# Performance work log

Measured on AMD Instinct MI355X. Metric: run time of the kernel, lower is better.

Reference implementation:

```python
import jax, jax.numpy as jnp
import numpy as np

B, L, D, V, K, H, HD, FFN = 64, 512, 256, 32000, 6, 4, 64, 512

def _ln(x, g, b):
    mu = x.mean(-1, keepdims=True)
    v = ((x - mu) ** 2).mean(-1, keepdims=True)
    return (x - mu) / jnp.sqrt(v + 1e-5) * g + b

def _pool(x, mask):
    # attention pooling: last real token attends over full sequence
    lengths = mask.sum(1)
    last = jnp.maximum(lengths - 1, 0)
    q = x[jnp.arange(x.shape[0]), last]                      # [B,D]
    scores = jnp.einsum('bd,bld->bl', q, x)
    scores = jnp.where(mask, scores, -60000.0)
    a = jax.nn.softmax(scores, axis=-1)
    return jnp.einsum('bl,bld->bd', a, x)

def _expert(x, mask, ln1g, ln1b, Wqkv, bqkv, Wo, bo, ln2g, ln2b, W1, b1, W2, b2):
    # pre-LN transformer block, eval mode (dropout = identity)
    Bx, Lx, _ = x.shape
    h = _ln(x, ln1g, ln1b)
    qkv = h @ Wqkv.T + bqkv                                   # [B,L,3D]
    q, k, v = jnp.split(qkv, 3, axis=-1)
    q = q.reshape(Bx, Lx, H, HD).transpose(0, 2, 1, 3)
    k = k.reshape(Bx, Lx, H, HD).transpose(0, 2, 1, 3)
    v = v.reshape(Bx, Lx, H, HD).transpose(0, 2, 1, 3)
    s = jnp.einsum('bhqd,bhkd->bhqk', q, k) / jnp.sqrt(jnp.float32(HD))
    s = jnp.where(mask[:, None, None, :], s, -1e9)            # key_padding_mask
    a = jax.nn.softmax(s, axis=-1)
    o = jnp.einsum('bhqk,bhkd->bhqd', a, v).transpose(0, 2, 1, 3).reshape(Bx, Lx, D)
    x = x + o @ Wo.T + bo
    h2 = _ln(x, ln2g, ln2b)
    ff = jax.nn.gelu(h2 @ W1.T + b1, approximate=False) @ W2.T + b2
    return x + ff

def _gru(z, m, Wih, Whh, bih, bhh):
    # torch.nn.GRUCell semantics
    gi = z @ Wih.T + bih
    gh = m @ Whh.T + bhh
    ir, iz, inn = jnp.split(gi, 3, axis=-1)
    hr, hz, hn = jnp.split(gh, 3, axis=-1)
    r = jax.nn.sigmoid(ir + hr)
    u = jax.nn.sigmoid(iz + hz)
    n = jnp.tanh(inn + r * hn)
    return (1.0 - u) * n + u * m

def setup_inputs():
    key = jax.random.key(0)
    ks = jax.random.split(key, 24)
    def nrm(k, shape, s=0.02):
        return jax.random.normal(k, shape, jnp.float32) * s
    lengths = jax.random.randint(ks[0], (B,), 1, L + 1)
    mask = jnp.arange(L)[None, :] < lengths[:, None]          # prefix mask, >=1 real token
    tokens = jnp.where(mask, jax.random.randint(ks[1], (B, L), 1, V), 0)
    return dict(
        tokens=tokens, mask=mask,
        tok_emb=nrm(ks[2], (V, D)).at[0].set(0.0),            # padding_idx=0
        pos_emb=nrm(ks[3], (L, D)),
        emb_ln_g=jnp.ones((D,)), emb_ln_b=jnp.zeros((D,)),
        ln1_g=jnp.ones((K, D)), ln1_b=jnp.zeros((K, D)),
        Wqkv=nrm(ks[4], (K, 3 * D, D)), bqkv=jnp.zeros((K, 3 * D)),
        Wo=nrm(ks[5], (K, D, D)), bo=jnp.zeros((K, D)),
        ln2_g=jnp.ones((K, D)), ln2_b=jnp.zeros((K, D)),
        W1=nrm(ks[6], (K, FFN, D)), b1=jnp.zeros((K, FFN)),
        W2=nrm(ks[7], (K, D, FFN)), b2=jnp.zeros((K, D)),
        gru_Wih=nrm(ks[8], (3 * D, D)), gru_Whh=nrm(ks[9], (3 * D, D)),
        gru_bih=jnp.zeros((3 * D,)), gru_bhh=jnp.zeros((3 * D,)),
        cls_W=nrm(ks[10], (V, D)), cls_b=jnp.zeros((V,)),
    )

def reference(tokens, mask, tok_emb, pos_emb, emb_ln_g, emb_ln_b, ln1_g, ln1_b, Wqkv, bqkv, Wo, bo, ln2_g, ln2_b, W1, b1, W2, b2, gru_Wih, gru_Whh, gru_bih, gru_bhh, cls_W, cls_b):
    x = _ln(tok_emb[tokens] + pos_emb[None, :tokens.shape[1]], emb_ln_g, emb_ln_b)
    m = jnp.zeros((tokens.shape[0], D), x.dtype)
    # sequential routing / phase-1: n_iter = K, chosen = t % K for all samples, no halting
    for t in range(K):
        e = t % K
        x = _expert(x, mask, ln1_g[e], ln1_b[e], Wqkv[e], bqkv[e], Wo[e], bo[e],
                    ln2_g[e], ln2_b[e], W1[e], b1[e], W2[e], b2[e])
        z = _pool(x, mask)
        m = _gru(z, m, gru_Wih, gru_Whh, gru_bih, gru_bhh)    # GRU memory update
    return _pool(x, mask) @ cls_W.T + cls_b                   # [B, V] logits
```

## Files before the change

### kernel.cpp

```cpp
#include <hip/hip_runtime.h>
#include <hip/hip_bf16.h>

#define BB 64
#define LL 512
#define DD 256
#define VV 32000
#define KK 6
#define HH 4
#define FF 512
#define MM (BB * LL)

typedef __hip_bfloat16 bf16;
typedef unsigned short ushort_t;
typedef __attribute__((ext_vector_type(8))) __bf16 bf16x8;
typedef __attribute__((ext_vector_type(4))) float f32x4;
#define MFMA __builtin_amdgcn_mfma_f32_16x16x32_bf16

__device__ __forceinline__ ushort_t f2bfbits(float x) {
  return __builtin_bit_cast(unsigned short, (__bf16)x);
}
__device__ __forceinline__ float bf2f(ushort_t u) {
  return __uint_as_float((unsigned)u << 16);
}
__device__ __forceinline__ unsigned pkbf(float lo, float hi) {
  return (unsigned)f2bfbits(lo) | ((unsigned)f2bfbits(hi) << 16);
}
union U8 { unsigned u[4]; bf16x8 v; };

__device__ __forceinline__ void gl_lds16(const ushort_t* g, ushort_t* l) {
  __builtin_amdgcn_global_load_lds(
      (const __attribute__((address_space(1))) unsigned int*)g,
      (__attribute__((address_space(3))) unsigned int*)l, 16, 0, 0);
}

__global__ __launch_bounds__(512) void k_lensord(const int* __restrict__ tokens,
                                                 int* __restrict__ lens,
                                                 int* __restrict__ order) {
  __shared__ int L[64];
  int t = threadIdx.x;
  int b = t >> 3, seg = t & 7;
  int c = 0;
  const int* tp = tokens + b * LL + seg * 64;
  #pragma unroll
  for (int i = 0; i < 64; i++) c += (tp[i] != 0);
  c += __shfl_down(c, 4, 64);
  c += __shfl_down(c, 2, 64);
  c += __shfl_down(c, 1, 64);
  if (seg == 0) { lens[b] = c; L[b] = c; }
  __syncthreads();
  if (t < 64) {
    int len = L[t];
    int rank = 0;
    for (int i = 0; i < 64; i++) {
      int li = L[i];
      if (li > len || (li == len && i < t)) rank++;
    }
    order[rank] = t;
  }
}

__global__ __launch_bounds__(256) void k_embed4(const int* __restrict__ tokens,
                                                const float* __restrict__ tok_emb,
                                                const float* __restrict__ pos_emb,
                                                const float* __restrict__ g,
                                                const float* __restrict__ be,
                                                const float* __restrict__ g1,
                                                const float* __restrict__ b1,
                                                ushort_t* __restrict__ X,
                                                bf16* __restrict__ H) {
  int wid = threadIdx.x >> 6, lane = threadIdx.x & 63;
  int row = blockIdx.x * 4 + wid;
  int l = row & (LL - 1);
  int tok = tokens[row];
  float4 a = *reinterpret_cast<const float4*>(tok_emb + (size_t)tok * DD + lane * 4);
  float4 p = *reinterpret_cast<const float4*>(pos_emb + (size_t)l * DD + lane * 4);
  float4 v = {a.x + p.x, a.y + p.y, a.z + p.z, a.w + p.w};
  float s = v.x + v.y + v.z + v.w;
  float q = v.x * v.x + v.y * v.y + v.z * v.z + v.w * v.w;
  #pragma unroll
  for (int o = 32; o > 0; o >>= 1) { s += __shfl_xor(s, o, 64); q += __shfl_xor(q, o, 64); }
  float mu = s * (1.f / DD);
  float rstd = rsqrtf(q * (1.f / DD) - mu * mu + 1e-5f);
  float4 gv = *reinterpret_cast<const float4*>(g + lane * 4);
  float4 bv = *reinterpret_cast<const float4*>(be + lane * 4);
  float4 o4 = {(v.x - mu) * rstd * gv.x + bv.x, (v.y - mu) * rstd * gv.y + bv.y,
               (v.z - mu) * rstd * gv.z + bv.z, (v.w - mu) * rstd * gv.w + bv.w};
  ushort4 x4;
  x4.x = f2bfbits(o4.x); x4.y = f2bfbits(o4.y); x4.z = f2bfbits(o4.z); x4.w = f2bfbits(o4.w);
  *reinterpret_cast<ushort4*>(X + (size_t)row * DD + lane * 4) = x4;
  float s2 = o4.x + o4.y + o4.z + o4.w;
  float q2 = o4.x * o4.x + o4.y * o4.y + o4.z * o4.z + o4.w * o4.w;
  #pragma unroll
  for (int o = 32; o > 0; o >>= 1) { s2 += __shfl_xor(s2, o, 64); q2 += __shfl_xor(q2, o, 64); }
  float mu2 = s2 * (1.f / DD);
  float rstd2 = rsqrtf(q2 * (1.f / DD) - mu2 * mu2 + 1e-5f);
  float4 g1v = *reinterpret_cast<const float4*>(g1 + lane * 4);
  float4 b1v = *reinterpret_cast<const float4*>(b1 + lane * 4);
  ushort4 h4;
  h4.x = f2bfbits((o4.x - mu2) * rstd2 * g1v.x + b1v.x);
  h4.y = f2bfbits((o4.y - mu2) * rstd2 * g1v.y + b1v.y);
  h4.z = f2bfbits((o4.z - mu2) * rstd2 * g1v.z + b1v.z);
  h4.w = f2bfbits((o4.w - mu2) * rstd2 * g1v.w + b1v.w);
  *reinterpret_cast<ushort4*>((ushort_t*)H + (size_t)row * DD + lane * 4) = h4;
}

__global__ __launch_bounds__(256) void k_cvtall(const float* __restrict__ Wqkv,
                                                const float* __restrict__ Wo,
                                                const float* __restrict__ W1,
                                                const float* __restrict__ W2,
                                                ushort_t* __restrict__ d) {
  int i = (blockIdx.x * 256 + threadIdx.x) * 4;
  int e = i / 524288, r = i - e * 524288;
  const float* s;
  if (r < 196608)      s = Wqkv + (size_t)e * 196608 + r;
  else if (r < 262144) s = Wo + (size_t)e * 65536 + (r - 196608);
  else if (r < 393216) s = W1 + (size_t)e * 131072 + (r - 262144);
  else                 s = W2 + (size_t)e * 131072 + (r - 393216);
  float4 v = *reinterpret_cast<const float4*>(s);
  ushort4 o;
  o.x = f2bfbits(v.x); o.y = f2bfbits(v.y); o.z = f2bfbits(v.z); o.w = f2bfbits(v.w);
  *reinterpret_cast<ushort4*>(d + i) = o;
}

template <int MT, int NT, int KD, bool GELU, bool RES, bool OUTBF16, bool FUSELN, bool QKVT>
__global__ __launch_bounds__(256) void k_mgemm(const ushort_t* __restrict__ A,
                                               const ushort_t* __restrict__ Wb,
                                               const float* __restrict__ bias,
                                               const ushort_t* __restrict__ res,
                                               void* __restrict__ outp,
                                               ushort_t* __restrict__ Hout,
                                               const float* __restrict__ lng,
                                               const float* __restrict__ lnb,
                                               const int* __restrict__ lens,
                                               int Ndim) {
  constexpr int JF = (MT == 128) ? (NT / 32) : (NT / 64);
  constexpr int AR = MT / 64, BR = NT / 64;
  constexpr int L = AR + BR;
  constexpr int NK = KD / 32;
  constexpr int ASZ = 3 * MT * 32;
  int n0 = blockIdx.x * NT, m0 = blockIdx.y * MT;
  if ((m0 & (LL - 1)) >= lens[m0 >> 9]) return;
  __shared__ __align__(16) ushort_t SH[ASZ + 3 * NT * 32];
  ushort_t* As = SH;
  ushort_t* Bs = SH + ASZ;
  int t = threadIdx.x, lane = t & 63, w = t >> 6;
  int wr = (MT == 128) ? (w >> 1) * 64 : 0;
  int wc = (MT == 128) ? (w & 1) * (NT / 2) : w * (NT / 4);
  int fr = lane & 15, fg = lane >> 4;

  int ca = lane & 3;
  const ushort_t* gA[AR];
  #pragma unroll
  for (int ra = 0; ra < AR; ra++) {
    int row = ra * 64 + (t >> 2);
    gA[ra] = A + (size_t)(m0 + row) * KD + ((ca ^ ((row >> 1) & 3)) << 3);
  }
  const ushort_t* gB[BR];
  #pragma unroll
  for (int rb = 0; rb < BR; rb++) {
    int row = rb * 64 + (t >> 2);
    gB[rb] = Wb + (size_t)(n0 + row) * KD + ((ca ^ ((row >> 1) & 3)) << 3);
  }

  f32x4 acc[4][JF];
  #pragma unroll
  for (int i = 0; i < 4; i++)
    #pragma unroll
    for (int j = 0; j < JF; j++) acc[i][j] = (f32x4){0.f, 0.f, 0.f, 0.f};

  #define STAGE(bi, koff) { \
    _Pragma("unroll") for (int ra = 0; ra < AR; ra++) gl_lds16(gA[ra] + (koff), &As[(bi) * MT * 32 + ra * 2048 + w * 512]); \
    _Pragma("unroll") for (int rb = 0; rb < BR; rb++) gl_lds16(gB[rb] + (koff), &Bs[(bi) * NT * 32 + rb * 2048 + w * 512]); }

  STAGE(0, 0);
  #pragma unroll
  for (int kt = 0; kt < NK; kt++) {
    int cur = kt % 3;
    if (kt + 1 < NK) {
      STAGE((kt + 1) % 3, (kt + 1) * 32);
      asm volatile("s_waitcnt vmcnt(%0)" :: "n"(L) : "memory");
    } else {
      asm volatile("s_waitcnt vmcnt(0)" ::: "memory");
    }
    __builtin_amdgcn_s_barrier();
    __builtin_amdgcn_sched_barrier(0);
    bf16x8 af[4], bfr[JF];
    #pragma unroll
    for (int i = 0; i < 4; i++) {
      int row = wr + i * 16 + fr;
      af[i] = *reinterpret_cast<const bf16x8*>(&As[cur * MT * 32 + row * 32 + ((fg ^ ((row >> 1) & 3)) << 3)]);
    }
    #pragma unroll
    for (int j = 0; j < JF; j++) {
      int row = wc + j * 16 + fr;
      bfr[j] = *reinterpret_cast<const bf16x8*>(&Bs[cur * NT * 32 + row * 32 + ((fg ^ ((row >> 1) & 3)) << 3)]);
    }
    #pragma unroll
    for (int i = 0; i < 4; i++)
      #pragma unroll
      for (int j = 0; j < JF; j++)
        acc[i][j] = MFMA(af[i], bfr[j], acc[i][j], 0, 0, 0);
  }
  #undef STAGE

  if constexpr (QKVT) {
    if (n0 < 512) {
      #pragma unroll
      for (int i = 0; i < 4; i++) {
        int mbase = m0 + wr + i * 16 + fg * 4;
        #pragma unroll
        for (int j = 0; j < JF; j++) {
          int n = n0 + wc + j * 16 + fr;
          float bs = bias[n];
          #pragma unroll
          for (int r = 0; r < 4; r++)
            ((ushort_t*)outp)[(size_t)(mbase + r) * 512 + n] = f2bfbits(acc[i][j][r] + bs);
        }
      }
    } else {
      __syncthreads();
      #pragma unroll
      for (int i = 0; i < 4; i++) {
        #pragma unroll
        for (int j = 0; j < JF; j++) {
          int dfull = wc + j * 16 + fr;
          float bs = bias[512 + dfull];
          int kl = wr + i * 16 + fg * 4;
          #pragma unroll
          for (int r = 0; r < 4; r++)
            SH[dfull * 136 + kl + r] = f2bfbits(acc[i][j][r] + bs);
        }
      }
      __syncthreads();
      int bidx = m0 >> 9, k0 = m0 & (LL - 1);
      #pragma unroll
      for (int it = 0; it < 16; it++) {
        int g = it * 256 + t;
        int row = g >> 4, mc = g & 15;
        uint4 val = *reinterpret_cast<const uint4*>(&SH[row * 136 + mc * 8]);
        *reinterpret_cast<uint4*>(Hout + (((size_t)(bidx * 4 + (row >> 6)) * 64 + (row & 63)) << 9) + k0 + mc * 8) = val;
      }
    }
  } else if constexpr (!FUSELN) {
    #pragma unroll
    for (int i = 0; i < 4; i++) {
      int mbase = m0 + wr + i * 16 + fg * 4;
      #pragma unroll
      for (int j = 0; j < JF; j++) {
        int n = n0 + wc + j * 16 + fr;
        float bs = bias[n];
        #pragma unroll
        for (int r = 0; r < 4; r++) {
          int m = mbase + r;
          float v = acc[i][j][r] + bs;
          if (RES) v += bf2f(res[(size_t)m * Ndim + n]);
          if (GELU) v = 0.5f * v * (1.f + erff(v * 0.70710678118f));
          if (OUTBF16) ((ushort_t*)outp)[(size_t)m * Ndim + n] = f2bfbits(v);
          else         ((float*)outp)[(size_t)m * Ndim + n] = v;
        }
      }
    }
  } else {
    __shared__ float redS[4][64], redQ[4][64], lnmv[64], lnrv[64];
    float rs[4][4], rq[4][4];
    #pragma unroll
    for (int i = 0; i < 4; i++)
      #pragma unroll
      for (int r = 0; r < 4; r++) { rs[i][r] = 0.f; rq[i][r] = 0.f; }
    #pragma unroll
    for (int i = 0; i < 4; i++) {
      #pragma unroll
      for (int j = 0; j < 4; j++) {
        int n = wc + j * 16 + fr;
        float bs = bias[n];
        #pragma unroll
        for (int r = 0; r < 4; r++) {
          int m = m0 + i * 16 + fg * 4 + r;
          float v = acc[i][j][r] + bs;
          if (RES) v += bf2f(res[(size_t)m * DD + n]);
          acc[i][j][r] = v;
          ((ushort_t*)outp)[(size_t)m * DD + n] = f2bfbits(v);
          rs[i][r] += v; rq[i][r] += v * v;
        }
      }
    }
    #pragma unroll
    for (int i = 0; i < 4; i++)
      #pragma unroll
      for (int r = 0; r < 4; r++) {
        float s = rs[i][r], q = rq[i][r];
        s += __shfl_xor(s, 1, 64); q += __shfl_xor(q, 1, 64);
        s += __shfl_xor(s, 2, 64); q += __shfl_xor(q, 2, 64);
        s += __shfl_xor(s, 4, 64); q += __shfl_xor(q, 4, 64);
        s += __shfl_xor(s, 8, 64); q += __shfl_xor(q, 8, 64);
        if (fr == 0) {
          redS[w][i * 16 + fg * 4 + r] = s;
          redQ[w][i * 16 + fg * 4 + r] = q;
        }
      }
    __syncthreads();
    if (t < 64) {
      float s = redS[0][t] + redS[1][t] + redS[2][t] + redS[3][t];
      float q = redQ[0][t] + redQ[1][t] + redQ[2][t] + redQ[3][t];
      float mu = s * (1.f / DD);
      lnmv[t] = mu;
      lnrv[t] = rsqrtf(q * (1.f / DD) - mu * mu + 1e-5f);
    }
    __syncthreads();
    #pragma unroll
    for (int i = 0; i < 4; i++) {
      #pragma unroll
      for (int j = 0; j < 4; j++) {
        int n = wc + j * 16 + fr;
        float gv = lng[n], bv = lnb[n];
        #pragma unroll
        for (int r = 0; r < 4; r++) {
          int rl = i * 16 + fg * 4 + r;
          float h = (acc[i][j][r] - lnmv[rl]) * lnrv[rl] * gv + bv;
          Hout[(size_t)(m0 + rl) * DD + n] = f2bfbits(h);
        }
      }
    }
  }
}

__global__ __launch_bounds__(512) void k_mattn10(const ushort_t* __restrict__ QK,
                                                 const ushort_t* __restrict__ VT,
                                                 const int* __restrict__ lens,
                                                 const int* __restrict__ order,
                                                 ushort_t* __restrict__ O) {
  int b = order[blockIdx.z], h = blockIdx.y;
  int len = lens[b];
  int q0 = blockIdx.x * 128;
  if (q0 >= len) return;
  int t = threadIdx.x, lane = t & 63, w = t >> 6;
  int fr = lane & 15, fg = lane >> 4;
  __shared__ __align__(16) ushort_t Kh[8192];
  __shared__ __align__(16) ushort_t Vh[8192];

  int qw = q0 + w * 16;
  bool qact = qw < len;
  int q = qw + fr;

  const ushort_t* qp = QK + (size_t)(b * LL + q) * 512 + h * 64 + fg * 8;
  bf16x8 qf0 = *reinterpret_cast<const bf16x8*>(qp);
  bf16x8 qf1 = *reinterpret_cast<const bf16x8*>(qp + 32);
  const ushort_t* vbase = VT + (((size_t)(b * 4 + h) * 64) << 9);

  const float SC = 0.125f * 1.44269504f;
  f32x4 ot[4];
  #pragma unroll
  for (int df = 0; df < 4; df++) ot[df] = (f32x4){0.f, 0.f, 0.f, 0.f};
  float lsum = 0.f;

  for (int kb = 0; kb < len; kb += 128) {
    if (kb) __syncthreads();
    int lim = min(128, len - kb);
    #pragma unroll
    for (int rr = 0; rr < 2; rr++) {
      if (rr * 64 >= lim) break;
      int krow = rr * 64 + w * 8 + (lane >> 3);
      int gk = kb + krow; if (gk > len - 1) gk = len - 1;
      int ch = lane & 7;
      const ushort_t* src = QK + (size_t)(b * LL + gk) * 512 + 256 + h * 64 + ((ch ^ (krow & 7)) << 3);
      gl_lds16(src, &Kh[rr * 4096 + w * 512]);
    }
    #pragma unroll
    for (int rr = 0; rr < 2; rr++) {
      int d = rr * 32 + w * 4 + (lane >> 4);
      int ch = lane & 15;
      int sd = (d ^ (d >> 3)) & 7;
      int chs = (ch & 8) | ((ch & 7) ^ sd);
      const ushort_t* src = vbase + ((size_t)d << 9) + kb + (chs << 3);
      gl_lds16(src, &Vh[rr * 4096 + w * 512]);
    }
    __syncthreads();

    if (qact) {
      for (int kt = 0; kt < lim; kt += 64) {
        f32x4 s[4];
        __builtin_amdgcn_s_setprio(1);
        #pragma unroll
        for (int f = 0; f < 4; f++) {
          s[f] = (f32x4){0.f, 0.f, 0.f, 0.f};
          int krow = kt + f * 16 + fr;
          const ushort_t* kp0 = &Kh[krow * 64 + ((fg ^ (krow & 7)) << 3)];
          const ushort_t* kp1 = &Kh[krow * 64 + (((4 + fg) ^ (krow & 7)) << 3)];
          s[f] = MFMA(*reinterpret_cast<const bf16x8*>(kp0), qf0, s[f], 0, 0, 0);
          s[f] = MFMA(*reinterpret_cast<const bf16x8*>(kp1), qf1, s[f], 0, 0, 0);
        }
        __builtin_amdgcn_s_setprio(0);
        float ps = 0.f;
        if (lim - kt >= 64) {
          #pragma unroll
          for (int f = 0; f < 4; f++)
            #pragma unroll
            for (int r = 0; r < 4; r++) {
              float p = exp2f(s[f][r] * SC);
              s[f][r] = p; ps += p;
            }
        } else {
          int rem = lim - kt;
          #pragma unroll
          for (int f = 0; f < 4; f++)
            #pragma unroll
            for (int r = 0; r < 4; r++) {
              float p = (f * 16 + fg * 4 + r < rem) ? exp2f(s[f][r] * SC) : 0.f;
              s[f][r] = p; ps += p;
            }
        }
        ps += __shfl_xor(ps, 16, 64);
        ps += __shfl_xor(ps, 32, 64);
        lsum += ps;
        #pragma unroll
        for (int st = 0; st < 2; st++) {
          int fA = st * 2, fB = fA + 1;
          unsigned a0 = pkbf(s[fA][0], s[fA][1]), a1 = pkbf(s[fA][2], s[fA][3]);
          unsigned b0 = pkbf(s[fB][0], s[fB][1]), b1 = pkbf(s[fB][2], s[fB][3]);
          int sA = ((fg & 1) * 2) * 16 + fr;
          int sB = sA + 16;
          unsigned wa0 = __shfl(a0, sA, 64), wb0 = __shfl(b0, sA, 64);
          unsigned wa1 = __shfl(a1, sA, 64), wb1 = __shfl(b1, sA, 64);
          unsigned wa2 = __shfl(a0, sB, 64), wb2 = __shfl(b0, sB, 64);
          unsigned wa3 = __shfl(a1, sB, 64), wb3 = __shfl(b1, sB, 64);
          bool lo = fg < 2;
          U8 pf;
          pf.u[0] = lo ? wa0 : wb0; pf.u[1] = lo ? wa1 : wb1;
          pf.u[2] = lo ? wa2 : wb2; pf.u[3] = lo ? wa3 : wb3;
          int cb = (kt >> 3) + st * 4 + fg;
          __builtin_amdgcn_s_setprio(1);
          #pragma unroll
          for (int df = 0; df < 4; df++) {
            int d = df * 16 + fr;
            int sd = (d ^ (d >> 3)) & 7;
            const ushort_t* vp = &Vh[d * 128 + ((cb ^ sd) << 3)];
            ot[df] = MFMA(*reinterpret_cast<const bf16x8*>(vp), pf.v, ot[df], 0, 0, 0);
          }
          __builtin_amdgcn_s_setprio(0);
        }
      }
    }
  }

  if (q < len) {
    float linv = 1.f / lsum;
    #pragma unroll
    for (int df = 0; df < 4; df++) {
      ushort4 ov;
      ov.x = f2bfbits(ot[df][0] * linv);
      ov.y = f2bfbits(ot[df][1] * linv);
      ov.z = f2bfbits(ot[df][2] * linv);
      ov.w = f2bfbits(ot[df][3] * linv);
      *reinterpret_cast<ushort4*>(O + (size_t)(b * LL + q) * DD + h * 64 + df * 16 + fg * 4) = ov;
    }
  }
}

__device__ __forceinline__ float blk_sum(float v, float* red) {
  #pragma unroll
  for (int o = 32; o > 0; o >>= 1) v += __shfl_down(v, o, 64);
  __syncthreads();
  if ((threadIdx.x & 63) == 0) red[threadIdx.x >> 6] = v;
  __syncthreads();
  return red[0] + red[1] + red[2] + red[3];
}

__global__ __launch_bounds__(256) void k_pool(const ushort_t* __restrict__ X,
                                              const int* __restrict__ lens,
                                              bf16* __restrict__ pooled) {
  __shared__ float red[4];
  __shared__ float qs[DD];
  __shared__ float sc[LL];
  int b = blockIdx.x, t = threadIdx.x;
  int len = lens[b];
  const ushort_t* Xb = X + (size_t)b * LL * DD;
  qs[t] = bf2f(Xb[(size_t)(len - 1) * DD + t]);
  __syncthreads();
  for (int l = t; l < LL; l += 256) {
    float s = -1e30f;
    if (l < len) {
      const ushort_t* xr = Xb + (size_t)l * DD;
      float a0 = 0.f;
      #pragma unroll
      for (int k8 = 0; k8 < 32; k8++) {
        uint4 xv = *reinterpret_cast<const uint4*>(xr + k8 * 8);
        const float* qq = qs + k8 * 8;
        a0 += bf2f((ushort_t)(xv.x & 0xffff)) * qq[0] + bf2f((ushort_t)(xv.x >> 16)) * qq[1];
        a0 += bf2f((ushort_t)(xv.y & 0xffff)) * qq[2] + bf2f((ushort_t)(xv.y >> 16)) * qq[3];
        a0 += bf2f((ushort_t)(xv.z & 0xffff)) * qq[4] + bf2f((ushort_t)(xv.z >> 16)) * qq[5];
        a0 += bf2f((ushort_t)(xv.w & 0xffff)) * qq[6] + bf2f((ushort_t)(xv.w >> 16)) * qq[7];
      }
      s = a0;
    }
    sc[l] = s;
  }
  __syncthreads();
  float mx = fmaxf(sc[t], sc[t + 256]);
  #pragma unroll
  for (int off = 32; off > 0; off >>= 1) mx = fmaxf(mx, __shfl_down(mx, off, 64));
  __syncthreads();
  if ((t & 63) == 0) red[t >> 6] = mx;
  __syncthreads();
  mx = fmaxf(fmaxf(red[0], red[1]), fmaxf(red[2], red[3]));
  float e0 = (t < len) ? __expf(sc[t] - mx) : 0.f;
  float e1 = (t + 256 < len) ? __expf(sc[t + 256] - mx) : 0.f;
  float ssum = blk_sum(e0 + e1, red);
  float inv = 1.f / ssum;
  __syncthreads();
  sc[t] = e0 * inv; sc[t + 256] = e1 * inv;
  __syncthreads();
  float acc = 0.f;
  for (int l = 0; l < len; l++) acc += sc[l] * bf2f(Xb[(size_t)l * DD + t]);
  pooled[b * DD + t] = __float2bfloat16(acc);
}

__global__ __launch_bounds__(512) void k_cls(const ushort_t* __restrict__ POOL,
                                             const float* __restrict__ W,
                                             const float* __restrict__ bias,
                                             float* __restrict__ out) {
  int t = threadIdx.x, lane = t & 63, w = t >> 6;
  int fr = lane & 15, fg = lane >> 4;
  int n = blockIdx.x * 128 + w * 16 + fr;
  const float* wp = W + (size_t)n * DD + fg * 8;
  f32x4 acc[4];
  #pragma unroll
  for (int i = 0; i < 4; i++) acc[i] = (f32x4){0.f, 0.f, 0.f, 0.f};
  for (int k0 = 0; k0 < DD; k0 += 32) {
    float4 f0 = *reinterpret_cast<const float4*>(wp + k0);
    float4 f1 = *reinterpret_cast<const float4*>(wp + k0 + 4);
    U8 bfr;
    bfr.u[0] = pkbf(f0.x, f0.y); bfr.u[1] = pkbf(f0.z, f0.w);
    bfr.u[2] = pkbf(f1.x, f1.y); bfr.u[3] = pkbf(f1.z, f1.w);
    #pragma unroll
    for (int i = 0; i < 4; i++) {
      bf16x8 af = *reinterpret_cast<const bf16x8*>(POOL + (size_t)(i * 16 + fr) * DD + k0 + fg * 8);
      acc[i] = MFMA(af, bfr.v, acc[i], 0, 0, 0);
    }
  }
  float bs = bias[n];
  #pragma unroll
  for (int i = 0; i < 4; i++)
    #pragma unroll
    for (int r = 0; r < 4; r++)
      out[(size_t)(i * 16 + fg * 4 + r) * VV + n] = acc[i][r] + bs;
}

extern "C" void kernel_launch(void* const* d_in, const int* in_sizes, int n_in,
                              void* d_out, int out_size, void* d_ws, size_t ws_size,
                              hipStream_t stream) {
  const int*   tokens  = (const int*)d_in[0];
  const float* tok_emb = (const float*)d_in[2];
  const float* pos_emb = (const float*)d_in[3];
  const float* emb_g   = (const float*)d_in[4];
  const float* emb_b   = (const float*)d_in[5];
  const float* ln1_g   = (const float*)d_in[6];
  const float* ln1_b   = (const float*)d_in[7];
  const float* Wqkv    = (const float*)d_in[8];
  const float* bqkv    = (const float*)d_in[9];
  const float* Wo      = (const float*)d_in[10];
  const float* bo      = (const float*)d_in[11];
  const float* ln2_g   = (const float*)d_in[12];
  const float* ln2_b   = (const float*)d_in[13];
  const float* W1      = (const float*)d_in[14];
  const float* b1      = (const float*)d_in[15];
  const float* W2      = (const float*)d_in[16];
  const float* b2      = (const float*)d_in[17];
  const float* cls_W   = (const float*)d_in[22];
  const float* cls_b   = (const float*)d_in[23];

  char* ws = (char*)d_ws;
  ushort_t* X    = (ushort_t*)ws;
  ushort_t* QKb  = (ushort_t*)(ws + 33554432);
  ushort_t* VTg  = (ushort_t*)(ws + 67108864);
  ushort_t* Hb   = (ushort_t*)(ws + 83886080);
  ushort_t* WB6  = (ushort_t*)(ws + 100663296);
  ushort_t* POOL = (ushort_t*)(ws + 106954752);
  int*      LEN  = (int*)(ws + 106987520);
  int*      ORD  = (int*)(ws + 106987776);

  const int OFF_QKV = 0, OFF_WO = 196608, OFF_W1 = 262144, OFF_W2 = 393216;
  const int LW = 524288;

  k_lensord<<<1, 512, 0, stream>>>(tokens, LEN, ORD);
  k_cvtall<<<3072, 256, 0, stream>>>(Wqkv, Wo, W1, W2, WB6);
  k_embed4<<<MM / 4, 256, 0, stream>>>(tokens, tok_emb, pos_emb, emb_g, emb_b,
                                       ln1_g, ln1_b, X, (bf16*)Hb);

  for (int e = 0; e < KK; e++) {
    const ushort_t* WB = WB6 + (size_t)e * LW;
    k_mgemm<128, 256, 256, false, false, true, false, true><<<dim3(3, 256), 256, 0, stream>>>(
        Hb, WB + OFF_QKV, bqkv + e * 3 * DD, nullptr, QKb, VTg, nullptr, nullptr, LEN, 3 * DD);
    k_mattn10<<<dim3(4, HH, BB), 512, 0, stream>>>(QKb, VTg, LEN, ORD, Hb);
    k_mgemm<64, 256, 256, false, true, false, true, false><<<dim3(1, 512), 256, 0, stream>>>(
        Hb, WB + OFF_WO, bo + e * DD, X, X, Hb, ln2_g + e * DD, ln2_b + e * DD, LEN, DD);
    k_mgemm<128, 256, 256, true, false, true, false, false><<<dim3(2, 256), 256, 0, stream>>>(
        Hb, WB + OFF_W1, b1 + e * FF, nullptr, QKb, nullptr, nullptr, nullptr, LEN, FF);
    if (e < KK - 1) {
      k_mgemm<64, 256, 512, false, true, false, true, false><<<dim3(1, 512), 256, 0, stream>>>(
          QKb, WB + OFF_W2, b2 + e * DD, X, X, Hb,
          ln1_g + (e + 1) * DD, ln1_b + (e + 1) * DD, LEN, DD);
    } else {
      k_mgemm<64, 256, 512, false, true, true, false, false><<<dim3(1, 512), 256, 0, stream>>>(
          QKb, WB + OFF_W2, b2 + e * DD, X, X, nullptr, nullptr, nullptr, LEN, DD);
    }
  }

  k_pool<<<BB, 256, 0, stream>>>(X, LEN, (bf16*)POOL);
  k_cls<<<dim3(VV / 128), 512, 0, stream>>>(POOL, cls_W, cls_b, (float*)d_out);
}
```

Before: 759.2 us.

## Triple-buffer K/V tiles in attention with async prefetch and single barrier

Restructures the attention kernel's key/value loading into 64-key chunks held in a three-slot LDS ring. The next chunk is prefetched with async global-to-LDS loads while the current one is computed, using explicit vmcnt waits and one barrier per chunk in place of two syncthreads per 128-key block. This aims to hide global load latency behind MFMA work. The cost is more barriers overall because chunks are smaller, and correctness relies on the hand-written waitcnt and on three buffers being enough to avoid write-after-read hazards.

```diff
diff --git a/kernel.cpp b/kernel.cpp
--- a/kernel.cpp
+++ b/kernel.cpp
@@ -324,7 +324,7 @@
   }
 }
 
-__global__ __launch_bounds__(512) void k_mattn10(const ushort_t* __restrict__ QK,
+__global__ __launch_bounds__(512) void k_mattn11(const ushort_t* __restrict__ QK,
                                                  const ushort_t* __restrict__ VT,
                                                  const int* __restrict__ lens,
                                                  const int* __restrict__ order,
@@ -335,8 +335,8 @@
   if (q0 >= len) return;
   int t = threadIdx.x, lane = t & 63, w = t >> 6;
   int fr = lane & 15, fg = lane >> 4;
-  __shared__ __align__(16) ushort_t Kh[8192];
-  __shared__ __align__(16) ushort_t Vh[8192];
+  __shared__ __align__(16) ushort_t Kh[3][4096];
+  __shared__ __align__(16) ushort_t Vh[3][4096];
 
   int qw = q0 + w * 16;
   bool qact = qw < len;
@@ -353,94 +353,94 @@
   for (int df = 0; df < 4; df++) ot[df] = (f32x4){0.f, 0.f, 0.f, 0.f};
   float lsum = 0.f;
 
-  for (int kb = 0; kb < len; kb += 128) {
-    if (kb) __syncthreads();
-    int lim = min(128, len - kb);
-    #pragma unroll
-    for (int rr = 0; rr < 2; rr++) {
-      if (rr * 64 >= lim) break;
-      int krow = rr * 64 + w * 8 + (lane >> 3);
-      int gk = kb + krow; if (gk > len - 1) gk = len - 1;
-      int ch = lane & 7;
-      const ushort_t* src = QK + (size_t)(b * LL + gk) * 512 + 256 + h * 64 + ((ch ^ (krow & 7)) << 3);
-      gl_lds16(src, &Kh[rr * 4096 + w * 512]);
-    }
-    #pragma unroll
-    for (int rr = 0; rr < 2; rr++) {
-      int d = rr * 32 + w * 4 + (lane >> 4);
-      int ch = lane & 15;
-      int sd = (d ^ (d >> 3)) & 7;
-      int chs = (ch & 8) | ((ch & 7) ^ sd);
-      const ushort_t* src = vbase + ((size_t)d << 9) + kb + (chs << 3);
-      gl_lds16(src, &Vh[rr * 4096 + w * 512]);
-    }
-    __syncthreads();
+  int srow = w * 8 + (lane >> 3);
+  int sch = lane & 7;
+  int ssd = (srow ^ (srow >> 3)) & 7;
+  #define STAGEA(bi, hi) { \
+    int kb_ = (hi) * 64; \
+    int gk_ = kb_ + srow; if (gk_ > len - 1) gk_ = len - 1; \
+    gl_lds16(QK + (size_t)(b * LL + gk_) * 512 + 256 + h * 64 + ((sch ^ (srow & 7)) << 3), \
+             &Kh[bi][w * 512]); \
+    gl_lds16(vbase + ((size_t)srow << 9) + kb_ + ((sch ^ ssd) << 3), \
+             &Vh[bi][w * 512]); }
+
+  int nh = (len + 63) >> 6;
+  STAGEA(0, 0);
+  for (int hi = 0; hi < nh; hi++) {
+    int bi = hi % 3;
+    if (hi + 1 < nh) {
+      STAGEA((hi + 1) % 3, hi + 1);
+      asm volatile("s_waitcnt vmcnt(2)" ::: "memory");
+    } else {
+      asm volatile("s_waitcnt vmcnt(0)" ::: "memory");
+    }
+    __builtin_amdgcn_s_barrier();
+    __builtin_amdgcn_sched_barrier(0);
 
     if (qact) {
-      for (int kt = 0; kt < lim; kt += 64) {
-        f32x4 s[4];
+      int lim = len - hi * 64; if (lim > 64) lim = 64;
+      f32x4 s[4];
+      __builtin_amdgcn_s_setprio(1);
+      #pragma unroll
+      for (int f = 0; f < 4; f++) {
+        s[f] = (f32x4){0.f, 0.f, 0.f, 0.f};
+        int krow = f * 16 + fr;
+        const ushort_t* kp0 = &Kh[bi][krow * 64 + ((fg ^ (krow & 7)) << 3)];
+        const ushort_t* kp1 = &Kh[bi][krow * 64 + (((4 + fg) ^ (krow & 7)) << 3)];
+        s[f] = MFMA(*reinterpret_cast<const bf16x8*>(kp0), qf0, s[f], 0, 0, 0);
+        s[f] = MFMA(*reinterpret_cast<const bf16x8*>(kp1), qf1, s[f], 0, 0, 0);
+      }
+      __builtin_amdgcn_s_setprio(0);
+      float ps = 0.f;
+      if (lim >= 64) {
+        #pragma unroll
+        for (int f = 0; f < 4; f++)
+          #pragma unroll
+          for (int r = 0; r < 4; r++) {
+            float p = exp2f(s[f][r] * SC);
+            s[f][r] = p; ps += p;
+          }
+      } else {
+        #pragma unroll
+        for (int f = 0; f < 4; f++)
+          #pragma unroll
+          for (int r = 0; r < 4; r++) {
+            float p = (f * 16 + fg * 4 + r < lim) ? exp2f(s[f][r] * SC) : 0.f;
+            s[f][r] = p; ps += p;
+          }
+      }
+      ps += __shfl_xor(ps, 16, 64);
+      ps += __shfl_xor(ps, 32, 64);
+      lsum += ps;
+      #pragma unroll
+      for (int st = 0; st < 2; st++) {
+        int fA = st * 2, fB = fA + 1;
+        unsigned a0 = pkbf(s[fA][0], s[fA][1]), a1 = pkbf(s[fA][2], s[fA][3]);
+        unsigned b0 = pkbf(s[fB][0], s[fB][1]), b1 = pkbf(s[fB][2], s[fB][3]);
+        int sA = ((fg & 1) * 2) * 16 + fr;
+        int sB = sA + 16;
+        unsigned wa0 = __shfl(a0, sA, 64), wb0 = __shfl(b0, sA, 64);
+        unsigned wa1 = __shfl(a1, sA, 64), wb1 = __shfl(b1, sA, 64);
+        unsigned wa2 = __shfl(a0, sB, 64), wb2 = __shfl(b0, sB, 64);
+        unsigned wa3 = __shfl(a1, sB, 64), wb3 = __shfl(b1, sB, 64);
+        bool lo = fg < 2;
+        U8 pf;
+        pf.u[0] = lo ? wa0 : wb0; pf.u[1] = lo ? wa1 : wb1;
+        pf.u[2] = lo ? wa2 : wb2; pf.u[3] = lo ? wa3 : wb3;
+        int cb = st * 4 + fg;
         __builtin_amdgcn_s_setprio(1);
         #pragma unroll
-        for (int f = 0; f < 4; f++) {
-          s[f] = (f32x4){0.f, 0.f, 0.f, 0.f};
-          int krow = kt + f * 16 + fr;
-          const ushort_t* kp0 = &Kh[krow * 64 + ((fg ^ (krow & 7)) << 3)];
-          const ushort_t* kp1 = &Kh[krow * 64 + (((4 + fg) ^ (krow & 7)) << 3)];
-          s[f] = MFMA(*reinterpret_cast<const bf16x8*>(kp0), qf0, s[f], 0, 0, 0);
-          s[f] = MFMA(*reinterpret_cast<const bf16x8*>(kp1), qf1, s[f], 0, 0, 0);
+        for (int df = 0; df < 4; df++) {
+          int d = df * 16 + fr;
+          int sd = (d ^ (d >> 3)) & 7;
+          const ushort_t* vp = &Vh[bi][d * 64 + ((cb ^ sd) << 3)];
+          ot[df] = MFMA(*reinterpret_cast<const bf16x8*>(vp), pf.v, ot[df], 0, 0, 0);
         }
         __builtin_amdgcn_s_setprio(0);
-        float ps = 0.f;
-        if (lim - kt >= 64) {
-          #pragma unroll
-          for (int f = 0; f < 4; f++)
-            #pragma unroll
-            for (int r = 0; r < 4; r++) {
-              float p = exp2f(s[f][r] * SC);
-              s[f][r] = p; ps += p;
-            }
-        } else {
-          int rem = lim - kt;
-          #pragma unroll
-          for (int f = 0; f < 4; f++)
-            #pragma unroll
-            for (int r = 0; r < 4; r++) {
-              float p = (f * 16 + fg * 4 + r < rem) ? exp2f(s[f][r] * SC) : 0.f;
-              s[f][r] = p; ps += p;
-            }
-        }
-        ps += __shfl_xor(ps, 16, 64);
-        ps += __shfl_xor(ps, 32, 64);
-        lsum += ps;
-        #pragma unroll
-        for (int st = 0; st < 2; st++) {
-          int fA = st * 2, fB = fA + 1;
-          unsigned a0 = pkbf(s[fA][0], s[fA][1]), a1 = pkbf(s[fA][2], s[fA][3]);
-          unsigned b0 = pkbf(s[fB][0], s[fB][1]), b1 = pkbf(s[fB][2], s[fB][3]);
-          int sA = ((fg & 1) * 2) * 16 + fr;
-          int sB = sA + 16;
-          unsigned wa0 = __shfl(a0, sA, 64), wb0 = __shfl(b0, sA, 64);
-          unsigned wa1 = __shfl(a1, sA, 64), wb1 = __shfl(b1, sA, 64);
-          unsigned wa2 = __shfl(a0, sB, 64), wb2 = __shfl(b0, sB, 64);
-          unsigned wa3 = __shfl(a1, sB, 64), wb3 = __shfl(b1, sB, 64);
-          bool lo = fg < 2;
-          U8 pf;
-          pf.u[0] = lo ? wa0 : wb0; pf.u[1] = lo ? wa1 : wb1;
-          pf.u[2] = lo ? wa2 : wb2; pf.u[3] = lo ? wa3 : wb3;
-          int cb = (kt >> 3) + st * 4 + fg;
-          __builtin_amdgcn_s_setprio(1);
-          #pragma unroll
-          for (int df = 0; df < 4; df++) {
-            int d = df * 16 + fr;
-            int sd = (d ^ (d >> 3)) & 7;
-            const ushort_t* vp = &Vh[d * 128 + ((cb ^ sd) << 3)];
-            ot[df] = MFMA(*reinterpret_cast<const bf16x8*>(vp), pf.v, ot[df], 0, 0, 0);
-          }
-          __builtin_amdgcn_s_setprio(0);
-        }
-      }
-    }
-  }
+      }
+    }
+  }
+  #undef STAGEA
 
   if (q < len) {
     float linv = 1.f / lsum;
@@ -590,7 +590,7 @@
     const ushort_t* WB = WB6 + (size_t)e * LW;
     k_mgemm<128, 256, 256, false, false, true, false, true><<<dim3(3, 256), 256, 0, stream>>>(
         Hb, WB + OFF_QKV, bqkv + e * 3 * DD, nullptr, QKb, VTg, nullptr, nullptr, LEN, 3 * DD);
-    k_mattn10<<<dim3(4, HH, BB), 512, 0, stream>>>(QKb, VTg, LEN, ORD, Hb);
+    k_mattn11<<<dim3(4, HH, BB), 512, 0, stream>>>(QKb, VTg, LEN, ORD, Hb);
     k_mgemm<64, 256, 256, false, true, false, true, false><<<dim3(1, 512), 256, 0, stream>>>(
         Hb, WB + OFF_WO, bo + e * DD, X, X, Hb, ln2_g + e * DD, ln2_b + e * DD, LEN, DD);
     k_mgemm<128, 256, 256, true, false, true, false, false><<<dim3(2, 256), 256, 0, stream>>>(
```

New measurement: 737.5 us, median of 2. -2.9%, faster.
